# Kernel tuning notes

Hardware: AMD Instinct MI355X
Metric: run time of the kernel (lower is better)

The kernel has to match this reference:

```python
import jax, jax.numpy as jnp
import numpy as np

INPUT_DIM = 128
OUTPUT_DIM = 256
BATCH = 4096

def setup_inputs() -> dict:
    key = jax.random.key(0)
    k_x, k_w1, k_b1, k_w2, k_b2 = jax.random.split(key, 5)
    d = INPUT_DIM
    h = 2 * OUTPUT_DIM
    x = jax.random.normal(k_x, (BATCH, d), dtype=jnp.float32)
    # Linear weights stored as [in, out]; scale ~ torch default init
    W1 = jax.random.uniform(k_w1, (d * d, h), dtype=jnp.float32, minval=-1, maxval=1) / np.sqrt(d * d)
    b1 = jax.random.uniform(k_b1, (h,), dtype=jnp.float32, minval=-1, maxval=1) / np.sqrt(d * d)
    W2 = jax.random.uniform(k_w2, (h, OUTPUT_DIM), dtype=jnp.float32, minval=-1, maxval=1) / np.sqrt(h)
    b2 = jax.random.uniform(k_b2, (OUTPUT_DIM,), dtype=jnp.float32, minval=-1, maxval=1) / np.sqrt(h)
    return {"x": x, "W1": W1, "b1": b1, "W2": W2, "b2": b2}

def reference(x, W1, b1, W2, b2):
    B, d = x.shape
    # torch bmm of the two expanded copies: tp[b,i,j] = sum_k x[b,i]*x[b,j] = d * x[b,i]*x[b,j]
    tp = jnp.asarray(d, x.dtype) * jnp.einsum('bi,bj->bij', x, x)  # [B, d, d]
    flat = tp.reshape(B, d * d)
    h = jax.nn.relu(flat @ W1 + b1)  # [B, 2*output_dim]
    return h @ W2 + b2               # [B, output_dim]
```

## Files before the change

kernel.cpp:

```cpp
#include <hip/hip_runtime.h>
#include <hip/hip_bf16.h>


typedef __attribute__((ext_vector_type(8))) short short8;
typedef __attribute__((ext_vector_type(4))) float floatx4;

__device__ __forceinline__ unsigned short f2bf(float f) {
    union { float f; unsigned int u; } v; v.f = f;
    unsigned int r = v.u + 0x7fffu + ((v.u >> 16) & 1u);
    return (unsigned short)(r >> 16);
}
__device__ __forceinline__ float bf2f(unsigned short b) {
    union { unsigned int u; float f; } v; v.u = ((unsigned int)b) << 16;
    return v.f;
}

__global__ __launch_bounds__(256) void pack_w1_kernel(
    const float* __restrict__ W1, unsigned short* __restrict__ W1Tp) {
    __shared__ float tile[64][65];
    const int k0 = blockIdx.x * 64;
    const int c0 = blockIdx.y * 64;
    const int tr = threadIdx.x >> 4;
    const int tc4 = (threadIdx.x & 15) * 4;
#pragma unroll
    for (int p = 0; p < 4; ++p) {
        int k = p * 16 + tr;
        float4 v = *(const float4*)(W1 + (long)(k0 + k) * 512 + c0 + tc4);
        tile[k][tc4 + 0] = v.x; tile[k][tc4 + 1] = v.y;
        tile[k][tc4 + 2] = v.z; tile[k][tc4 + 3] = v.w;
    }
    __syncthreads();
    const int lane = threadIdx.x & 63;
    const int w = threadIdx.x >> 6;
    const int m = lane & 15, quad = lane >> 4;
#pragma unroll
    for (int pass = 0; pass < 2; ++pass) {
        int chunk = w * 2 + pass;
        int kcL = chunk & 1, c16L = chunk >> 1;
        union { unsigned short s[8]; uint4 u; } o;
#pragma unroll
        for (int j = 0; j < 8; ++j)
            o.s[j] = f2bf(tile[kcL * 32 + quad * 8 + j][c16L * 16 + m]);
        long c16g = (c0 >> 4) + c16L;
        long kcg  = (k0 >> 5) + kcL;
        *(uint4*)(W1Tp + (c16g * 512 + kcg) * 512 + lane * 8) = o.u;
    }
}

__global__ __launch_bounds__(256) void transpose_cast_kernel(
    const float* __restrict__ in, unsigned short* __restrict__ out, int R, int C) {
    __shared__ float tile[64][65];
    const int r0 = blockIdx.x * 64, c0 = blockIdx.y * 64;
    const int tr = threadIdx.x >> 4;
    const int tc4 = (threadIdx.x & 15) * 4;
#pragma unroll
    for (int p = 0; p < 4; ++p) {
        int r = p * 16 + tr;
        float4 v = *(const float4*)(in + (long)(r0 + r) * C + c0 + tc4);
        tile[r][tc4 + 0] = v.x; tile[r][tc4 + 1] = v.y;
        tile[r][tc4 + 2] = v.z; tile[r][tc4 + 3] = v.w;
    }
    __syncthreads();
#pragma unroll
    for (int p = 0; p < 4; ++p) {
        int c = p * 16 + tr;
        union { unsigned short s[4]; uint2 u; } pk;
#pragma unroll
        for (int e = 0; e < 4; ++e) pk.s[e] = f2bf(tile[tc4 + e][c]);
        *(uint2*)(out + (long)(c0 + c) * R + r0 + tc4) = pk.u;
    }
}


#define A_STEP(Ac00, Ac01, Ac10, Ac11, I)                                  \
    {                                                                      \
        float xi[8];                                                       \
        _Pragma("unroll")                                                  \
        for (int tn = 0; tn < 8; ++tn)                                     \
            xi[tn] = xT[bLloc + tn * 16][(I)];                             \
        _Pragma("unroll")                                                  \
        for (int tn = 0; tn < 8; ++tn) {                                   \
            floatx4 t0 = __builtin_amdgcn_mfma_f32_16x16x32_bf16(          \
                Ac00, Xf[0][tn], zero4, 0, 0, 0);                          \
            t0 = __builtin_amdgcn_mfma_f32_16x16x32_bf16(                  \
                Ac01, Xf[1][tn], t0, 0, 0, 0);                             \
            acc[0][tn] += xi[tn] * t0;                                     \
            floatx4 t1 = __builtin_amdgcn_mfma_f32_16x16x32_bf16(          \
                Ac10, Xf[0][tn], zero4, 0, 0, 0);                          \
            t1 = __builtin_amdgcn_mfma_f32_16x16x32_bf16(                  \
                Ac11, Xf[1][tn], t1, 0, 0, 0);                             \
            acc[1][tn] += xi[tn] * t1;                                     \
        }                                                                  \
        const int p_ = ((I) + 4) & 31;     \
        Ac00 = *(const short8*)(aB00 + (long)p_ * 2048);                   \
        Ac01 = *(const short8*)(aB01 + (long)p_ * 2048);                   \
        Ac10 = *(const short8*)(aB10 + (long)p_ * 2048);                   \
        Ac11 = *(const short8*)(aB11 + (long)p_ * 2048);                   \
    }

__global__ __launch_bounds__(256, 2) void gemm1_kernel(
    const float* __restrict__ x,
    const unsigned short* __restrict__ W1Tp,
    unsigned short* __restrict__ Pb) {
    __shared__ float xT[256][34];
    const int tid = threadIdx.x;
    const int n = blockIdx.x;
    const int L = (n & 7) * 64 + (n >> 3);
    const int b0 = (L & 15) * 256;
    const int c0 = ((L >> 4) & 7) * 64;
    const int zi = L >> 7;
    const int i0 = zi * 32;

    for (int idx = tid; idx < 256 * 32; idx += 256) {
        int bL = idx >> 5, iL = idx & 31;
        xT[bL][iL] = x[(long)(b0 + bL) * 128 + i0 + iL];
    }
    __syncthreads();

    const int wid = tid >> 6;
    const int wm = wid >> 1, wn = wid & 1;
    const int lane = tid & 63;
    const int n16 = lane & 15, quad = lane >> 4;
    const int bBase = b0 + wn * 128;
    const int c16base = (c0 >> 4) + wm * 2;
    const int bLloc = wn * 128 + n16;

    floatx4 acc[2][8];
#pragma unroll
    for (int tm = 0; tm < 2; ++tm)
#pragma unroll
        for (int tn = 0; tn < 8; ++tn) acc[tm][tn] = (floatx4){0.f, 0.f, 0.f, 0.f};
    const floatx4 zero4 = (floatx4){0.f, 0.f, 0.f, 0.f};

#pragma unroll
    for (int jh = 0; jh < 2; ++jh) {
        short8 Xf[2][8];
#pragma unroll
        for (int ks = 0; ks < 2; ++ks)
#pragma unroll
            for (int tn = 0; tn < 8; ++tn) {
                const float* xp = x + (long)(bBase + tn * 16 + n16) * 128
                                    + jh * 64 + ks * 32 + quad * 8;
                float4 v0 = *(const float4*)xp;
                float4 v1 = *(const float4*)(xp + 4);
                short8 f;
                f[0] = (short)f2bf(v0.x); f[1] = (short)f2bf(v0.y);
                f[2] = (short)f2bf(v0.z); f[3] = (short)f2bf(v0.w);
                f[4] = (short)f2bf(v1.x); f[5] = (short)f2bf(v1.y);
                f[6] = (short)f2bf(v1.z); f[7] = (short)f2bf(v1.w);
                Xf[ks][tn] = f;
            }
        const unsigned short* aB00 = W1Tp
            + ((long)(c16base + 0) * 512 + (long)i0 * 4 + jh * 2 + 0) * 512
            + lane * 8;
        const unsigned short* aB01 = aB00 + 512;
        const unsigned short* aB10 = W1Tp
            + ((long)(c16base + 1) * 512 + (long)i0 * 4 + jh * 2 + 0) * 512
            + lane * 8;
        const unsigned short* aB11 = aB10 + 512;

        short8 A0_00 = *(const short8*)(aB00);
        short8 A0_01 = *(const short8*)(aB01);
        short8 A0_10 = *(const short8*)(aB10);
        short8 A0_11 = *(const short8*)(aB11);
        short8 A1_00 = *(const short8*)(aB00 + 1 * 2048);
        short8 A1_01 = *(const short8*)(aB01 + 1 * 2048);
        short8 A1_10 = *(const short8*)(aB10 + 1 * 2048);
        short8 A1_11 = *(const short8*)(aB11 + 1 * 2048);
        short8 A2_00 = *(const short8*)(aB00 + 2 * 2048);
        short8 A2_01 = *(const short8*)(aB01 + 2 * 2048);
        short8 A2_10 = *(const short8*)(aB10 + 2 * 2048);
        short8 A2_11 = *(const short8*)(aB11 + 2 * 2048);
        short8 A3_00 = *(const short8*)(aB00 + 3 * 2048);
        short8 A3_01 = *(const short8*)(aB01 + 3 * 2048);
        short8 A3_10 = *(const short8*)(aB10 + 3 * 2048);
        short8 A3_11 = *(const short8*)(aB11 + 3 * 2048);

#pragma unroll 1
        for (int ib = 0; ib < 8; ++ib) {
            const int i = ib * 4;
            A_STEP(A0_00, A0_01, A0_10, A0_11, i + 0)
            A_STEP(A1_00, A1_01, A1_10, A1_11, i + 1)
            A_STEP(A2_00, A2_01, A2_10, A2_11, i + 2)
            A_STEP(A3_00, A3_01, A3_10, A3_11, i + 3)
        }
    }

    unsigned short* pb = Pb + (long)zi * (4096L * 512);
#pragma unroll
    for (int tm = 0; tm < 2; ++tm)
#pragma unroll
        for (int tn = 0; tn < 8; ++tn) {
            int b = bBase + tn * 16 + n16;
            int cb = (c16base + tm) * 16 + quad * 4;
            union { unsigned short s[4]; uint2 u; } pk;
#pragma unroll
            for (int r = 0; r < 4; ++r) pk.s[r] = f2bf(acc[tm][tn][r]);
            *(uint2*)(pb + (long)b * 512 + cb) = pk.u;
        }
}

__global__ __launch_bounds__(256) void tail_kernel(
    const unsigned short* __restrict__ Pb,
    const float* __restrict__ b1,
    const unsigned short* __restrict__ W2T,
    const float* __restrict__ b2,
    float* __restrict__ out) {
    __shared__ unsigned short hL[16][516];
    __shared__ float b1s[512];
    const int tid = threadIdx.x;
    const int b0 = blockIdx.x * 16;
    b1s[tid] = b1[tid];
    b1s[tid + 256] = b1[tid + 256];
    __syncthreads();

    const unsigned int* Pu = (const unsigned int*)Pb;
#pragma unroll 4
    for (int idx = tid; idx < 16 * 256; idx += 256) {
        int bL = idx >> 8;
        int cu = idx & 255;
        float s0 = 0.f, s1 = 0.f;
#pragma unroll
        for (int z = 0; z < 4; ++z) {
            unsigned int u = Pu[((long)z * 4096 + b0 + bL) * 256 + cu];
            s0 += bf2f((unsigned short)(u & 0xffff));
            s1 += bf2f((unsigned short)(u >> 16));
        }
        int c = cu * 2;
        float v0 = fmaxf(fmaf(128.f, s0, b1s[c]), 0.f);
        float v1 = fmaxf(fmaf(128.f, s1, b1s[c + 1]), 0.f);
        unsigned int pk = (unsigned int)f2bf(v0) | ((unsigned int)f2bf(v1) << 16);
        *(unsigned int*)&hL[bL][c] = pk;
    }
    __syncthreads();

    const int w = tid >> 6, lane = tid & 63;
    const int n16 = lane & 15, quad = lane >> 4;
    const int o0 = w * 64;
    floatx4 acc[4];
#pragma unroll
    for (int tn = 0; tn < 4; ++tn) acc[tn] = (floatx4){0.f, 0.f, 0.f, 0.f};

#pragma unroll 4
    for (int ks = 0; ks < 16; ++ks) {
        short8 Af, Bf[4];
        {
            const unsigned short* p = &hL[n16][ks * 32 + quad * 8];
            union { uint2 u[2]; short8 s; } cvt;
            cvt.u[0] = *(const uint2*)p;
            cvt.u[1] = *(const uint2*)(p + 4);
            Af = cvt.s;
        }
#pragma unroll
        for (int tn = 0; tn < 4; ++tn)
            Bf[tn] = *(const short8*)(W2T + (long)(o0 + tn * 16 + n16) * 512
                                      + ks * 32 + quad * 8);
#pragma unroll
        for (int tn = 0; tn < 4; ++tn)
            acc[tn] = __builtin_amdgcn_mfma_f32_16x16x32_bf16(
                Af, Bf[tn], acc[tn], 0, 0, 0);
    }
#pragma unroll
    for (int tn = 0; tn < 4; ++tn) {
        float bias = b2[o0 + tn * 16 + n16];
#pragma unroll
        for (int r = 0; r < 4; ++r)
            out[(long)(b0 + quad * 4 + r) * 256
                + o0 + tn * 16 + n16] = acc[tn][r] + bias;
    }
}

extern "C" void kernel_launch(void* const* d_in, const int* in_sizes, int n_in,
                              void* d_out, int out_size, void* d_ws, size_t ws_size,
                              hipStream_t stream) {
    const float* x  = (const float*)d_in[0];
    const float* W1 = (const float*)d_in[1];
    const float* b1 = (const float*)d_in[2];
    const float* W2 = (const float*)d_in[3];
    const float* b2 = (const float*)d_in[4];
    float* out = (float*)d_out;

    char* ws = (char*)d_ws;
    unsigned short* W1Tp = (unsigned short*)(ws);
    unsigned short* W2T  = (unsigned short*)(ws + 16777216);
    unsigned short* Pb   = (unsigned short*)(ws + 16777216 + 262144);

    pack_w1_kernel<<<dim3(256, 8), 256, 0, stream>>>(W1, W1Tp);
    transpose_cast_kernel<<<dim3(8, 4), 256, 0, stream>>>(W2, W2T, 512, 256);
    gemm1_kernel<<<dim3(512), 256, 0, stream>>>(x, W1Tp, Pb);
    tail_kernel<<<dim3(256), 256, 0, stream>>>(Pb, b1, W2T, b2, out);
}
```

Measured before the change: 175.7 us.

## Fold x_i scaling into bf16 B operand and accumulate directly in MFMA

Instead of computing per-i partial MFMA results from zero and scaling them into the accumulator with vector FMAs, the kernel now scales the x_j operand by x_i in fp32, packs it to bf16 with v_cvt_pk_bf16_f32, and accumulates straight into acc through the MFMA chain. The per-block batch tile is halved to 128 rows, the grid is doubled to 1024 blocks, and the A-fragment prefetch depth is cut from 4 to 2, reducing register pressure. The trade-off is extra scaling and convert instructions per step, plus a different rounding point, since the product x_i*x_j is now rounded to bf16.

Measured after the change: 181.0 us. 1.03x slower.

```diff
diff --git a/kernel.cpp b/kernel.cpp
--- a/kernel.cpp
+++ b/kernel.cpp
@@ -72,26 +72,41 @@
 }
 
 
-#define A_STEP(Ac00, Ac01, Ac10, Ac11, I)                                  \
+#define SCALEB(dst, XI, ks, tn)                                            \
     {                                                                      \
-        float xi[8];                                                       \
+        union { unsigned int u[4]; short8 s; } r_;                         \
         _Pragma("unroll")                                                  \
-        for (int tn = 0; tn < 8; ++tn)                                     \
-            xi[tn] = xT[bLloc + tn * 16][(I)];                             \
-        _Pragma("unroll")                                                  \
-        for (int tn = 0; tn < 8; ++tn) {                                   \
-            floatx4 t0 = __builtin_amdgcn_mfma_f32_16x16x32_bf16(          \
-                Ac00, Xf[0][tn], zero4, 0, 0, 0);                          \
-            t0 = __builtin_amdgcn_mfma_f32_16x16x32_bf16(                  \
-                Ac01, Xf[1][tn], t0, 0, 0, 0);                             \
-            acc[0][tn] += xi[tn] * t0;                                     \
-            floatx4 t1 = __builtin_amdgcn_mfma_f32_16x16x32_bf16(          \
-                Ac10, Xf[0][tn], zero4, 0, 0, 0);                          \
-            t1 = __builtin_amdgcn_mfma_f32_16x16x32_bf16(                  \
-                Ac11, Xf[1][tn], t1, 0, 0, 0);                             \
-            acc[1][tn] += xi[tn] * t1;                                     \
+        for (int p_ = 0; p_ < 4; ++p_) {                                   \
+            float lo_ = (XI) * xjF[ks][tn][2 * p_];                        \
+            float hi_ = (XI) * xjF[ks][tn][2 * p_ + 1];                    \
+            asm("v_cvt_pk_bf16_f32 %0, %1, %2"                             \
+                : "=v"(r_.u[p_]) : "v"(lo_), "v"(hi_));                    \
         }                                                                  \
-        const int p_ = ((I) + 4) & 31;     \
+        dst = r_.s;                                                        \
+    }
+
+#define MM(tm, tn, Aks0, Aks1, B0, B1)                                     \
+    acc[tm][tn] = __builtin_amdgcn_mfma_f32_16x16x32_bf16(                 \
+        Aks0, B0, acc[tm][tn], 0, 0, 0);                                   \
+    acc[tm][tn] = __builtin_amdgcn_mfma_f32_16x16x32_bf16(                 \
+        Aks1, B1, acc[tm][tn], 0, 0, 0);
+
+#define A_STEP(Ac00, Ac01, Ac10, Ac11, XI0, XI1, XI2, XI3, I)              \
+    {                                                                      \
+        short8 Bs00, Bs01, Bs02, Bs03, Bs10, Bs11, Bs12, Bs13;             \
+        SCALEB(Bs00, XI0, 0, 0) SCALEB(Bs01, XI1, 0, 1)                    \
+        SCALEB(Bs02, XI2, 0, 2) SCALEB(Bs03, XI3, 0, 3)                    \
+        SCALEB(Bs10, XI0, 1, 0) SCALEB(Bs11, XI1, 1, 1)                    \
+        SCALEB(Bs12, XI2, 1, 2) SCALEB(Bs13, XI3, 1, 3)                    \
+        MM(0, 0, Ac00, Ac01, Bs00, Bs10)                                   \
+        MM(0, 1, Ac00, Ac01, Bs01, Bs11)                                   \
+        MM(0, 2, Ac00, Ac01, Bs02, Bs12)                                   \
+        MM(0, 3, Ac00, Ac01, Bs03, Bs13)                                   \
+        MM(1, 0, Ac10, Ac11, Bs00, Bs10)                                   \
+        MM(1, 1, Ac10, Ac11, Bs01, Bs11)                                   \
+        MM(1, 2, Ac10, Ac11, Bs02, Bs12)                                   \
+        MM(1, 3, Ac10, Ac11, Bs03, Bs13)                                   \
+        const int p_ = ((I) + 2) & 31;     \
         Ac00 = *(const short8*)(aB00 + (long)p_ * 2048);                   \
         Ac01 = *(const short8*)(aB01 + (long)p_ * 2048);                   \
         Ac10 = *(const short8*)(aB10 + (long)p_ * 2048);                   \
@@ -102,16 +117,16 @@
     const float* __restrict__ x,
     const unsigned short* __restrict__ W1Tp,
     unsigned short* __restrict__ Pb) {
-    __shared__ float xT[256][34];
+    __shared__ float xT[128][34];
     const int tid = threadIdx.x;
     const int n = blockIdx.x;
-    const int L = (n & 7) * 64 + (n >> 3);
-    const int b0 = (L & 15) * 256;
-    const int c0 = ((L >> 4) & 7) * 64;
-    const int zi = L >> 7;
+    const int L = (n & 7) * 128 + (n >> 3);
+    const int b0 = (L & 31) * 128;
+    const int c0 = ((L >> 5) & 7) * 64;
+    const int zi = L >> 8;
     const int i0 = zi * 32;
 
-    for (int idx = tid; idx < 256 * 32; idx += 256) {
+    for (int idx = tid; idx < 128 * 32; idx += 256) {
         int bL = idx >> 5, iL = idx & 31;
         xT[bL][iL] = x[(long)(b0 + bL) * 128 + i0 + iL];
     }
@@ -121,34 +136,34 @@
     const int wm = wid >> 1, wn = wid & 1;
     const int lane = tid & 63;
     const int n16 = lane & 15, quad = lane >> 4;
-    const int bBase = b0 + wn * 128;
+    const int bBase = b0 + wn * 64;
     const int c16base = (c0 >> 4) + wm * 2;
-    const int bLloc = wn * 128 + n16;
-
-    floatx4 acc[2][8];
+    const int xrow0 = wn * 64 + n16;
+    const int xrow1 = xrow0 + 16;
+    const int xrow2 = xrow0 + 32;
+    const int xrow3 = xrow0 + 48;
+
+    floatx4 acc[2][4];
 #pragma unroll
     for (int tm = 0; tm < 2; ++tm)
 #pragma unroll
-        for (int tn = 0; tn < 8; ++tn) acc[tm][tn] = (floatx4){0.f, 0.f, 0.f, 0.f};
-    const floatx4 zero4 = (floatx4){0.f, 0.f, 0.f, 0.f};
+        for (int tn = 0; tn < 4; ++tn) acc[tm][tn] = (floatx4){0.f, 0.f, 0.f, 0.f};
 
 #pragma unroll
     for (int jh = 0; jh < 2; ++jh) {
-        short8 Xf[2][8];
+        float xjF[2][4][8];
 #pragma unroll
         for (int ks = 0; ks < 2; ++ks)
 #pragma unroll
-            for (int tn = 0; tn < 8; ++tn) {
+            for (int tn = 0; tn < 4; ++tn) {
                 const float* xp = x + (long)(bBase + tn * 16 + n16) * 128
                                     + jh * 64 + ks * 32 + quad * 8;
                 float4 v0 = *(const float4*)xp;
                 float4 v1 = *(const float4*)(xp + 4);
-                short8 f;
-                f[0] = (short)f2bf(v0.x); f[1] = (short)f2bf(v0.y);
-                f[2] = (short)f2bf(v0.z); f[3] = (short)f2bf(v0.w);
-                f[4] = (short)f2bf(v1.x); f[5] = (short)f2bf(v1.y);
-                f[6] = (short)f2bf(v1.z); f[7] = (short)f2bf(v1.w);
-                Xf[ks][tn] = f;
+                xjF[ks][tn][0] = v0.x; xjF[ks][tn][1] = v0.y;
+                xjF[ks][tn][2] = v0.z; xjF[ks][tn][3] = v0.w;
+                xjF[ks][tn][4] = v1.x; xjF[ks][tn][5] = v1.y;
+                xjF[ks][tn][6] = v1.z; xjF[ks][tn][7] = v1.w;
             }
         const unsigned short* aB00 = W1Tp
             + ((long)(c16base + 0) * 512 + (long)i0 * 4 + jh * 2 + 0) * 512
@@ -163,26 +178,22 @@
         short8 A0_01 = *(const short8*)(aB01);
         short8 A0_10 = *(const short8*)(aB10);
         short8 A0_11 = *(const short8*)(aB11);
-        short8 A1_00 = *(const short8*)(aB00 + 1 * 2048);
-        short8 A1_01 = *(const short8*)(aB01 + 1 * 2048);
-        short8 A1_10 = *(const short8*)(aB10 + 1 * 2048);
-        short8 A1_11 = *(const short8*)(aB11 + 1 * 2048);
-        short8 A2_00 = *(const short8*)(aB00 + 2 * 2048);
-        short8 A2_01 = *(const short8*)(aB01 + 2 * 2048);
-        short8 A2_10 = *(const short8*)(aB10 + 2 * 2048);
-        short8 A2_11 = *(const short8*)(aB11 + 2 * 2048);
-        short8 A3_00 = *(const short8*)(aB00 + 3 * 2048);
-        short8 A3_01 = *(const short8*)(aB01 + 3 * 2048);
-        short8 A3_10 = *(const short8*)(aB10 + 3 * 2048);
-        short8 A3_11 = *(const short8*)(aB11 + 3 * 2048);
+        short8 A1_00 = *(const short8*)(aB00 + 2048);
+        short8 A1_01 = *(const short8*)(aB01 + 2048);
+        short8 A1_10 = *(const short8*)(aB10 + 2048);
+        short8 A1_11 = *(const short8*)(aB11 + 2048);
 
 #pragma unroll 1
-        for (int ib = 0; ib < 8; ++ib) {
-            const int i = ib * 4;
-            A_STEP(A0_00, A0_01, A0_10, A0_11, i + 0)
-            A_STEP(A1_00, A1_01, A1_10, A1_11, i + 1)
-            A_STEP(A2_00, A2_01, A2_10, A2_11, i + 2)
-            A_STEP(A3_00, A3_01, A3_10, A3_11, i + 3)
+        for (int ib = 0; ib < 16; ++ib) {
+            const int i = ib * 2;
+            float2 xi0p = *(const float2*)&xT[xrow0][i];
+            float2 xi1p = *(const float2*)&xT[xrow1][i];
+            float2 xi2p = *(const float2*)&xT[xrow2][i];
+            float2 xi3p = *(const float2*)&xT[xrow3][i];
+            A_STEP(A0_00, A0_01, A0_10, A0_11,
+                   xi0p.x, xi1p.x, xi2p.x, xi3p.x, i)
+            A_STEP(A1_00, A1_01, A1_10, A1_11,
+                   xi0p.y, xi1p.y, xi2p.y, xi3p.y, i + 1)
         }
     }
 
@@ -190,7 +201,7 @@
 #pragma unroll
     for (int tm = 0; tm < 2; ++tm)
 #pragma unroll
-        for (int tn = 0; tn < 8; ++tn) {
+        for (int tn = 0; tn < 4; ++tn) {
             int b = bBase + tn * 16 + n16;
             int cb = (c16base + tm) * 16 + quad * 4;
             union { unsigned short s[4]; uint2 u; } pk;
@@ -287,6 +298,6 @@
 
     pack_w1_kernel<<<dim3(256, 8), 256, 0, stream>>>(W1, W1Tp);
     transpose_cast_kernel<<<dim3(8, 4), 256, 0, stream>>>(W2, W2T, 512, 256);
-    gemm1_kernel<<<dim3(512), 256, 0, stream>>>(x, W1Tp, Pb);
+    gemm1_kernel<<<dim3(1024), 256, 0, stream>>>(x, W1Tp, Pb);
     tail_kernel<<<dim3(256), 256, 0, stream>>>(Pb, b1, W2T, b2, out);
 }
```

## Merge weight prep kernels and store gemm1 partials in MFMA-tile layout

Applied to the files above, without the earlier changes.

The two weight preparation kernels (W1 pack and W2 transpose-cast) become one launch, with block index ranges choosing the task, which saves one kernel launch. gemm1 now writes its partial sums in a tile-blocked layout in which each lane's four bf16 values sit contiguously per 16x16 tile. The tail kernel reads this layout with one coalesced 8-byte load per lane per split and reduces four columns at once. The aim is cheaper partial-sum stores and reads than the earlier strided row-major scatter, at the cost of coupling the two kernels to this tile layout.

Result: faster. 170.3 us (-3.1%).

```diff
diff --git a/kernel.cpp b/kernel.cpp
--- a/kernel.cpp
+++ b/kernel.cpp
@@ -15,59 +15,59 @@
     return v.f;
 }
 
-__global__ __launch_bounds__(256) void pack_w1_kernel(
-    const float* __restrict__ W1, unsigned short* __restrict__ W1Tp) {
+__global__ __launch_bounds__(256) void prep_kernel(
+    const float* __restrict__ W1, unsigned short* __restrict__ W1Tp,
+    const float* __restrict__ W2, unsigned short* __restrict__ W2T) {
     __shared__ float tile[64][65];
-    const int k0 = blockIdx.x * 64;
-    const int c0 = blockIdx.y * 64;
+    const int blk = blockIdx.x;
     const int tr = threadIdx.x >> 4;
     const int tc4 = (threadIdx.x & 15) * 4;
-#pragma unroll
-    for (int p = 0; p < 4; ++p) {
-        int k = p * 16 + tr;
-        float4 v = *(const float4*)(W1 + (long)(k0 + k) * 512 + c0 + tc4);
-        tile[k][tc4 + 0] = v.x; tile[k][tc4 + 1] = v.y;
-        tile[k][tc4 + 2] = v.z; tile[k][tc4 + 3] = v.w;
-    }
-    __syncthreads();
-    const int lane = threadIdx.x & 63;
-    const int w = threadIdx.x >> 6;
-    const int m = lane & 15, quad = lane >> 4;
-#pragma unroll
-    for (int pass = 0; pass < 2; ++pass) {
-        int chunk = w * 2 + pass;
-        int kcL = chunk & 1, c16L = chunk >> 1;
-        union { unsigned short s[8]; uint4 u; } o;
-#pragma unroll
-        for (int j = 0; j < 8; ++j)
-            o.s[j] = f2bf(tile[kcL * 32 + quad * 8 + j][c16L * 16 + m]);
-        long c16g = (c0 >> 4) + c16L;
-        long kcg  = (k0 >> 5) + kcL;
-        *(uint4*)(W1Tp + (c16g * 512 + kcg) * 512 + lane * 8) = o.u;
-    }
-}
-
-__global__ __launch_bounds__(256) void transpose_cast_kernel(
-    const float* __restrict__ in, unsigned short* __restrict__ out, int R, int C) {
-    __shared__ float tile[64][65];
-    const int r0 = blockIdx.x * 64, c0 = blockIdx.y * 64;
-    const int tr = threadIdx.x >> 4;
-    const int tc4 = (threadIdx.x & 15) * 4;
-#pragma unroll
-    for (int p = 0; p < 4; ++p) {
-        int r = p * 16 + tr;
-        float4 v = *(const float4*)(in + (long)(r0 + r) * C + c0 + tc4);
-        tile[r][tc4 + 0] = v.x; tile[r][tc4 + 1] = v.y;
-        tile[r][tc4 + 2] = v.z; tile[r][tc4 + 3] = v.w;
-    }
-    __syncthreads();
-#pragma unroll
-    for (int p = 0; p < 4; ++p) {
-        int c = p * 16 + tr;
-        union { unsigned short s[4]; uint2 u; } pk;
-#pragma unroll
-        for (int e = 0; e < 4; ++e) pk.s[e] = f2bf(tile[tc4 + e][c]);
-        *(uint2*)(out + (long)(c0 + c) * R + r0 + tc4) = pk.u;
+    if (blk < 2048) {
+        const int k0 = (blk & 255) * 64;
+        const int c0 = (blk >> 8) * 64;
+#pragma unroll
+        for (int p = 0; p < 4; ++p) {
+            int k = p * 16 + tr;
+            float4 v = *(const float4*)(W1 + (long)(k0 + k) * 512 + c0 + tc4);
+            tile[k][tc4 + 0] = v.x; tile[k][tc4 + 1] = v.y;
+            tile[k][tc4 + 2] = v.z; tile[k][tc4 + 3] = v.w;
+        }
+        __syncthreads();
+        const int lane = threadIdx.x & 63;
+        const int w = threadIdx.x >> 6;
+        const int m = lane & 15, quad = lane >> 4;
+#pragma unroll
+        for (int pass = 0; pass < 2; ++pass) {
+            int chunk = w * 2 + pass;
+            int kcL = chunk & 1, c16L = chunk >> 1;
+            union { unsigned short s[8]; uint4 u; } o;
+#pragma unroll
+            for (int j = 0; j < 8; ++j)
+                o.s[j] = f2bf(tile[kcL * 32 + quad * 8 + j][c16L * 16 + m]);
+            long c16g = (c0 >> 4) + c16L;
+            long kcg  = (k0 >> 5) + kcL;
+            *(uint4*)(W1Tp + (c16g * 512 + kcg) * 512 + lane * 8) = o.u;
+        }
+    } else {
+        const int t = blk - 2048;
+        const int r0 = (t & 7) * 64, c0 = (t >> 3) * 64;
+        const int R = 512, C = 256;
+#pragma unroll
+        for (int p = 0; p < 4; ++p) {
+            int r = p * 16 + tr;
+            float4 v = *(const float4*)(W2 + (long)(r0 + r) * C + c0 + tc4);
+            tile[r][tc4 + 0] = v.x; tile[r][tc4 + 1] = v.y;
+            tile[r][tc4 + 2] = v.z; tile[r][tc4 + 3] = v.w;
+        }
+        __syncthreads();
+#pragma unroll
+        for (int p = 0; p < 4; ++p) {
+            int c = p * 16 + tr;
+            union { unsigned short s[4]; uint2 u; } pk;
+#pragma unroll
+            for (int e = 0; e < 4; ++e) pk.s[e] = f2bf(tile[tc4 + e][c]);
+            *(uint2*)(W2T + (long)(c0 + c) * R + r0 + tc4) = pk.u;
+        }
     }
 }
 
@@ -91,7 +91,7 @@
                 Ac11, Xf[1][tn], t1, 0, 0, 0);                             \
             acc[1][tn] += xi[tn] * t1;                                     \
         }                                                                  \
-        const int p_ = ((I) + 4) & 31;     \
+        const int p_ = ((I) + 4) & 31;  \
         Ac00 = *(const short8*)(aB00 + (long)p_ * 2048);                   \
         Ac01 = *(const short8*)(aB01 + (long)p_ * 2048);                   \
         Ac10 = *(const short8*)(aB10 + (long)p_ * 2048);                   \
@@ -186,17 +186,17 @@
         }
     }
 
-    unsigned short* pb = Pb + (long)zi * (4096L * 512);
 #pragma unroll
     for (int tm = 0; tm < 2; ++tm)
 #pragma unroll
         for (int tn = 0; tn < 8; ++tn) {
-            int b = bBase + tn * 16 + n16;
-            int cb = (c16base + tm) * 16 + quad * 4;
+            int ct = c16base + tm;
+            int bt = (bBase >> 4) + tn;
             union { unsigned short s[4]; uint2 u; } pk;
 #pragma unroll
             for (int r = 0; r < 4; ++r) pk.s[r] = f2bf(acc[tm][tn][r]);
-            *(uint2*)(pb + (long)b * 512 + cb) = pk.u;
+            *(uint2*)(Pb + (((long)(zi * 32 + ct) * 256 + bt) * 64 + lane) * 4)
+                = pk.u;
         }
 }
 
@@ -209,33 +209,39 @@
     __shared__ unsigned short hL[16][516];
     __shared__ float b1s[512];
     const int tid = threadIdx.x;
-    const int b0 = blockIdx.x * 16;
+    const int bt = blockIdx.x;
     b1s[tid] = b1[tid];
     b1s[tid + 256] = b1[tid + 256];
     __syncthreads();
 
-    const unsigned int* Pu = (const unsigned int*)Pb;
-#pragma unroll 4
-    for (int idx = tid; idx < 16 * 256; idx += 256) {
-        int bL = idx >> 8;
-        int cu = idx & 255;
-        float s0 = 0.f, s1 = 0.f;
-#pragma unroll
-        for (int z = 0; z < 4; ++z) {
-            unsigned int u = Pu[((long)z * 4096 + b0 + bL) * 256 + cu];
-            s0 += bf2f((unsigned short)(u & 0xffff));
-            s1 += bf2f((unsigned short)(u >> 16));
-        }
-        int c = cu * 2;
-        float v0 = fmaxf(fmaf(128.f, s0, b1s[c]), 0.f);
-        float v1 = fmaxf(fmaf(128.f, s1, b1s[c + 1]), 0.f);
-        unsigned int pk = (unsigned int)f2bf(v0) | ((unsigned int)f2bf(v1) << 16);
-        *(unsigned int*)&hL[bL][c] = pk;
-    }
-    __syncthreads();
-
     const int w = tid >> 6, lane = tid & 63;
     const int n16 = lane & 15, quad = lane >> 4;
+
+#pragma unroll
+    for (int cc = 0; cc < 8; ++cc) {
+        const int ct = cc * 4 + w;
+        float s0 = 0.f, s1 = 0.f, s2 = 0.f, s3 = 0.f;
+#pragma unroll
+        for (int z = 0; z < 4; ++z) {
+            uint2 u = *(const uint2*)(Pb
+                + (((long)(z * 32 + ct) * 256 + bt) * 64 + lane) * 4);
+            s0 += bf2f((unsigned short)(u.x & 0xffff));
+            s1 += bf2f((unsigned short)(u.x >> 16));
+            s2 += bf2f((unsigned short)(u.y & 0xffff));
+            s3 += bf2f((unsigned short)(u.y >> 16));
+        }
+        const int c = ct * 16 + quad * 4;
+        float v0 = fmaxf(fmaf(128.f, s0, b1s[c + 0]), 0.f);
+        float v1 = fmaxf(fmaf(128.f, s1, b1s[c + 1]), 0.f);
+        float v2 = fmaxf(fmaf(128.f, s2, b1s[c + 2]), 0.f);
+        float v3 = fmaxf(fmaf(128.f, s3, b1s[c + 3]), 0.f);
+        union { unsigned short s[4]; uint2 u; } pk;
+        pk.s[0] = f2bf(v0); pk.s[1] = f2bf(v1);
+        pk.s[2] = f2bf(v2); pk.s[3] = f2bf(v3);
+        *(uint2*)&hL[n16][c] = pk.u;
+    }
+    __syncthreads();
+
     const int o0 = w * 64;
     floatx4 acc[4];
 #pragma unroll
@@ -265,7 +271,7 @@
         float bias = b2[o0 + tn * 16 + n16];
 #pragma unroll
         for (int r = 0; r < 4; ++r)
-            out[(long)(b0 + quad * 4 + r) * 256
+            out[(long)(bt * 16 + quad * 4 + r) * 256
                 + o0 + tn * 16 + n16] = acc[tn][r] + bias;
     }
 }
@@ -285,8 +291,7 @@
     unsigned short* W2T  = (unsigned short*)(ws + 16777216);
     unsigned short* Pb   = (unsigned short*)(ws + 16777216 + 262144);
 
-    pack_w1_kernel<<<dim3(256, 8), 256, 0, stream>>>(W1, W1Tp);
-    transpose_cast_kernel<<<dim3(8, 4), 256, 0, stream>>>(W2, W2T, 512, 256);
+    prep_kernel<<<dim3(2080), 256, 0, stream>>>(W1, W1Tp, W2, W2T);
     gemm1_kernel<<<dim3(512), 256, 0, stream>>>(x, W1Tp, Pb);
     tail_kernel<<<dim3(256), 256, 0, stream>>>(Pb, b1, W2T, b2, out);
 }
```
